# Optimization experiments

Measured on AMD Instinct MI355X. Metric: run time of the kernel, lower is better.

## Reference

```python
import jax, jax.numpy as jnp
import numpy as np

B, M, N, C, D, H, TOPK = 32, 20000, 500000, 128, 128, 4, 100
EPS = 1e-5


def setup_inputs() -> dict:
    key = jax.random.key(0)
    ks = jax.random.split(key, 24)
    f = lambda k, s: jax.random.normal(k, s, dtype=jnp.float32) * 0.05
    inp = {
        'lhs_embedding': f(ks[0], (B, C)),
        'rhs_gnn_embedding': f(ks[1], (M, C)),
        'rhs_emb_weight': f(ks[2], (N, D)),
        'proj_W': f(ks[3], (D, C)), 'proj_b': jnp.zeros((D,), jnp.float32),
        'head_W': f(ks[4], (1, C)), 'head_b': jnp.zeros((1,), jnp.float32),
        'off_emb_W': f(ks[5], (1, D)), 'off_emb_b': jnp.zeros((1,), jnp.float32),
        'off_id_W': f(ks[6], (1, D)), 'off_id_b': jnp.zeros((1,), jnp.float32),
        'Wq': f(ks[7], (D, D)), 'bq': jnp.zeros((D,), jnp.float32),
        'Wk': f(ks[8], (D, D)), 'bk': jnp.zeros((D,), jnp.float32),
        'Wv': f(ks[9], (D, D)), 'bv': jnp.zeros((D,), jnp.float32),
        'Wo': f(ks[10], (D, D)), 'bo': jnp.zeros((D,), jnp.float32),
        'ln1_g': jnp.ones((D,), jnp.float32), 'ln1_b': jnp.zeros((D,), jnp.float32),
        'ffn_W': f(ks[11], (D, D)), 'ffn_b': jnp.zeros((D,), jnp.float32),
        'ln2_g': jnp.ones((D,), jnp.float32), 'ln2_b': jnp.zeros((D,), jnp.float32),
        'rhs_idgnn_index': jax.random.randint(ks[12], (M,), 0, N, dtype=jnp.int32),
        'lhs_idgnn_batch': jnp.sort(jax.random.randint(ks[13], (M,), 0, B, dtype=jnp.int32)),
    }
    return inp


def _ln(x, g, b):
    mu = jnp.mean(x, axis=-1, keepdims=True)
    var = jnp.mean(jnp.square(x - mu), axis=-1, keepdims=True)
    return (x - mu) * jax.lax.rsqrt(var + EPS) * g + b


def reference(lhs_embedding, rhs_gnn_embedding, rhs_emb_weight, proj_W, proj_b,
              head_W, head_b, off_emb_W, off_emb_b, off_id_W, off_id_b,
              Wq, bq, Wk, bk, Wv, bv, Wo, bo, ln1_g, ln1_b, ffn_W, ffn_b,
              ln2_g, ln2_b, rhs_idgnn_index, lhs_idgnn_batch):
    # --- embgnn logits: dense [B,N] matmul + per-row offset ---
    lhs_proj = lhs_embedding @ proj_W.T + proj_b                          # [B,D]
    embgnn_logits = lhs_proj @ rhs_emb_weight.T                           # [B,N]
    embgnn_logits = embgnn_logits + (lhs_proj @ off_emb_W[0] + off_emb_b[0])[:, None]

    # --- idgnn logits on sampled rhs nodes ---
    idgnn_logits = rhs_gnn_embedding @ head_W[0] + head_b[0]              # [M]
    idgnn_logits = idgnn_logits + jnp.sum(lhs_embedding[lhs_idgnn_batch] * rhs_gnn_embedding, axis=-1)
    idgnn_offset = lhs_proj @ off_id_W[0] + off_id_b[0]                   # [B]
    idgnn_logits = idgnn_logits + idgnn_offset[lhs_idgnn_batch]

    # scatter idgnn logits into the dense logits tensor
    embgnn_logits = embgnn_logits.at[lhs_idgnn_batch, rhs_idgnn_index].set(idgnn_logits)

    # --- final rhs embeddings: shallow table + scattered GNN embeddings ---
    copy_tensor = jnp.zeros_like(rhs_emb_weight).at[rhs_idgnn_index].set(rhs_gnn_embedding)
    final_rhs_embed = rhs_emb_weight + copy_tensor                        # [N,D]

    # --- rerank: topk -> gather -> MAB -> scatter back ---
    _, topk_index = jax.lax.top_k(embgnn_logits, TOPK)                    # [B,TOPK]
    top_embed = final_rhs_embed[topk_index]                               # [B,TOPK,D]

    dh = D // H
    q = (top_embed @ Wq.T + bq).reshape(B, TOPK, H, dh)
    k = (top_embed @ Wk.T + bk).reshape(B, TOPK, H, dh)
    v = (top_embed @ Wv.T + bv).reshape(B, TOPK, H, dh)
    att = jnp.einsum('bthd,bshd->bhts', q, k) / jnp.sqrt(jnp.float32(dh))
    att = jax.nn.softmax(att, axis=-1)
    o = jnp.einsum('bhts,bshd->bthd', att, v).reshape(B, TOPK, D) @ Wo.T + bo
    x = _ln(top_embed + o, ln1_g, ln1_b)
    x = _ln(x + jax.nn.relu(x @ ffn_W.T + ffn_b), ln2_g, ln2_b)           # tr_embed [B,TOPK,D]

    # original code passes lhs_proj[lhs_idgnn_batch] and indexes rows 0..B-1
    lhs_q = lhs_proj[lhs_idgnn_batch][:B]                                 # [B,D]
    scores = jnp.sum(lhs_q[:, None, :] * x, axis=-1)                      # [B,TOPK]
    rows = jnp.arange(B)[:, None]
    transformer_logits = jnp.full((B, N), -jnp.inf, dtype=embgnn_logits.dtype)
    transformer_logits = transformer_logits.at[rows, topk_index].set(scores)

    return embgnn_logits, transformer_logits, topk_index
```

## Files before the change

kernel.cpp:

```cpp
#include <hip/hip_runtime.h>

typedef unsigned long long u64;
typedef unsigned int u32;

#define N_NODES 500000
#define M_SAMP  20000
#define BB      32
#define DD      128
#define TOPK    100
#define NBINS   2048
#define CAP     2048
#define C4PB    3907
#define LN_EPS  1e-5f
#define NEG_BIG -1.0e30f

__device__ __forceinline__ u32 fkey(float x) {
  u32 u = __float_as_uint(x);
  u32 mask = (u32)((int)u >> 31) | 0x80000000u;
  return u ^ mask;
}

__global__ void k_lhsproj(const float* __restrict__ lhs, const float* __restrict__ pW,
                          const float* __restrict__ pb, const float* __restrict__ oeW,
                          const float* __restrict__ oeb, const float* __restrict__ oiW,
                          const float* __restrict__ oib,
                          float* __restrict__ lhs_proj, float* __restrict__ lhs_projT,
                          float* __restrict__ oe_sc, float* __restrict__ oi_sc) {
  __shared__ float lrow[DD];
  __shared__ float red[DD];
  int b = blockIdx.x, d = threadIdx.x;
  lrow[d] = lhs[b * DD + d];
  __syncthreads();
  float acc = pb[d];
  for (int c = 0; c < DD; ++c) acc += lrow[c] * pW[d * DD + c];
  lhs_proj[b * DD + d] = acc;
  lhs_projT[d * BB + b] = acc;
  red[d] = acc * oeW[d];
  __syncthreads();
  for (int s = 64; s > 0; s >>= 1) { if (d < s) red[d] += red[d + s]; __syncthreads(); }
  if (d == 0) oe_sc[b] = red[0] + oeb[0];
  __syncthreads();
  red[d] = acc * oiW[d];
  __syncthreads();
  for (int s = 64; s > 0; s >>= 1) { if (d < s) red[d] += red[d + s]; __syncthreads(); }
  if (d == 0) oi_sc[b] = red[0] + oib[0];
}

__global__ void k_idgnn(const float* __restrict__ rgnn, const float* __restrict__ lhs,
                        const float* __restrict__ hW, const float* __restrict__ hb,
                        const float* __restrict__ oi_sc,
                        const int* __restrict__ ridx, const int* __restrict__ rbat,
                        float* __restrict__ val, int* __restrict__ win) {
  int wid = threadIdx.x >> 6, lane = threadIdx.x & 63;
  int m = blockIdx.x * 4 + wid;
  if (m >= M_SAMP) return;
  int b = rbat[m], n = ridx[m];
  float2 rg = ((const float2*)(rgnn + (size_t)m * DD))[lane];
  float2 hw = ((const float2*)hW)[lane];
  float2 le = ((const float2*)(lhs + (size_t)b * DD))[lane];
  float p = rg.x * hw.x + rg.y * hw.y + rg.x * le.x + rg.y * le.y;
  for (int off = 32; off > 0; off >>= 1) p += __shfl_down(p, off);
  int w = 1;
  for (int j0 = m + 1; j0 < M_SAMP; j0 += 64) {
    int j = j0 + lane;
    bool inb = (j < M_SAMP) && (rbat[j] == b);
    bool match = inb && (ridx[j] == n);
    if (__ballot(match)) { w = 0; break; }
    if (__ballot(inb) != ~0ULL) break;
  }
  if (lane == 0) { val[m] = p + hb[0] + oi_sc[b]; win[m] = w; }
}

__global__ void k_setup(int* __restrict__ inv, u32* __restrict__ hist,
                        u32* __restrict__ cand_cnt) {
  int i = blockIdx.x * 256 + threadIdx.x;
  if (i < N_NODES) inv[i] = -1;
  if (i < BB * NBINS) hist[i] = 0;
  if (i < BB) cand_cnt[i] = 0;
}

__global__ __launch_bounds__(256) void k_embgnn(const float* __restrict__ rhs,
    const float* __restrict__ lhsT, const float* __restrict__ oe_sc,
    float* __restrict__ out, float* __restrict__ tr) {
  __shared__ float sT[64][DD + 4];
  int tid = threadIdx.x;
  long n0 = (long)blockIdx.x * 64;
  #pragma unroll
  for (int p = 0; p < 8; ++p) {
    int f = p * 256 + tid;
    int r = f >> 5, c4 = (f & 31) << 2;
    long n = n0 + r; if (n >= N_NODES) n = N_NODES - 1;
    float4 v = *(const float4*)(rhs + n * DD + c4);
    sT[r][c4] = v.x; sT[r][c4 + 1] = v.y; sT[r][c4 + 2] = v.z; sT[r][c4 + 3] = v.w;
  }
  __syncthreads();
  int lane = tid & 63;
  int bg = __builtin_amdgcn_readfirstlane((tid >> 6) * 8);
  float acc[8];
  #pragma unroll
  for (int j = 0; j < 8; ++j) acc[j] = 0.f;
  const float4* srow = (const float4*)&sT[lane][0];
  #pragma unroll 4
  for (int cq = 0; cq < 32; ++cq) {
    float4 rv = srow[cq];
    const float* lp = lhsT + cq * 4 * BB + bg;
    #pragma unroll
    for (int j = 0; j < 8; ++j) {
      acc[j] += lp[j] * rv.x;
      acc[j] += lp[BB + j] * rv.y;
      acc[j] += lp[2 * BB + j] * rv.z;
      acc[j] += lp[3 * BB + j] * rv.w;
    }
  }
  long n = n0 + lane;
  if (n < N_NODES) {
    #pragma unroll
    for (int j = 0; j < 8; ++j) {
      out[(long)(bg + j) * N_NODES + n] = acc[j] + oe_sc[bg + j];
      tr[(long)(bg + j) * N_NODES + n] = NEG_BIG;
    }
  }
}

__global__ void k_scatter2(const int* __restrict__ ridx, const int* __restrict__ rbat,
                           const float* __restrict__ val, const int* __restrict__ win,
                           int* __restrict__ inv, float* __restrict__ out) {
  int m = blockIdx.x * 256 + threadIdx.x;
  if (m < M_SAMP) {
    atomicMax(&inv[ridx[m]], m);
    if (win[m]) out[(long)rbat[m] * N_NODES + ridx[m]] = val[m];
  }
}

__global__ void k_hist(const float* __restrict__ out, u32* __restrict__ hist) {
  __shared__ u32 hsh[NBINS];
  int tid = threadIdx.x;
  for (int i = tid; i < NBINS; i += 256) hsh[i] = 0;
  __syncthreads();
  int row = blockIdx.y;
  const float4* o4 = (const float4*)out + (long)row * (N_NODES / 4);
  int start = blockIdx.x * C4PB;
  int end = min(start + C4PB, N_NODES / 4);
  for (int i = start + tid; i < end; i += 256) {
    float4 v = o4[i];
    atomicAdd(&hsh[fkey(v.x) >> 21], 1u);
    atomicAdd(&hsh[fkey(v.y) >> 21], 1u);
    atomicAdd(&hsh[fkey(v.z) >> 21], 1u);
    atomicAdd(&hsh[fkey(v.w) >> 21], 1u);
  }
  __syncthreads();
  for (int i = tid; i < NBINS; i += 256)
    if (hsh[i]) atomicAdd(&hist[row * NBINS + i], hsh[i]);
}

__global__ void k_collect(const float* __restrict__ out, const u32* __restrict__ hist,
                          u32* __restrict__ cand_cnt, u64* __restrict__ cand) {
  __shared__ u32 part[256];
  __shared__ int s_cb;
  int tid = threadIdx.x, row = blockIdx.y;
  const u32* hrow = hist + row * NBINS;
  u32 p = 0;
  #pragma unroll
  for (int j = 0; j < 8; ++j) p += hrow[tid * 8 + j];
  part[tid] = p;
  __syncthreads();
  if (tid == 0) {
    u32 cum = 0; int g = 255, found = 0;
    for (; g > 0; --g) { cum += part[g]; if (cum >= TOPK) { found = 1; break; } }
    u32 c2 = found ? (cum - part[g]) : cum;
    int hi = found ? g * 8 + 7 : 7;
    int bin;
    for (bin = hi; bin > 0; --bin) { c2 += hrow[bin]; if (c2 >= TOPK) break; }
    s_cb = bin;
  }
  __syncthreads();
  u32 cb = (u32)s_cb;
  const float4* o4 = (const float4*)out + (long)row * (N_NODES / 4);
  int start = blockIdx.x * C4PB;
  int end = min(start + C4PB, N_NODES / 4);
  for (int i = start + tid; i < end; i += 256) {
    float4 v = o4[i];
    u32 kk[4] = { fkey(v.x), fkey(v.y), fkey(v.z), fkey(v.w) };
    #pragma unroll
    for (int j = 0; j < 4; ++j) {
      if ((kk[j] >> 21) >= cb) {
        u32 pos = atomicAdd(&cand_cnt[row], 1u);
        int idx = i * 4 + j;
        if (pos < CAP) cand[(long)row * CAP + pos] = ((u64)kk[j] << 32) | (u32)(~idx);
      }
    }
  }
}

__global__ __launch_bounds__(1024) void k_sort(const u64* __restrict__ cand,
                                               const u32* __restrict__ cand_cnt,
                                               int* __restrict__ topk_out) {
  __shared__ u64 sh[CAP];
  int row = blockIdx.x, tid = threadIdx.x;
  int cnt = min((int)cand_cnt[row], CAP);
  int NS = 128; while (NS < cnt) NS <<= 1;
  for (int i = tid; i < NS; i += 1024) sh[i] = (i < cnt) ? cand[(long)row * CAP + i] : 0ULL;
  __syncthreads();
  for (int k2 = 2; k2 <= NS; k2 <<= 1) {
    for (int j = k2 >> 1; j > 0; j >>= 1) {
      for (int i = tid; i < NS; i += 1024) {
        int ixj = i ^ j;
        if (ixj > i) {
          u64 a = sh[i], c = sh[ixj];
          bool up = ((i & k2) == 0);
          if (up ? (a < c) : (a > c)) { sh[i] = c; sh[ixj] = a; }
        }
      }
      __syncthreads();
    }
  }
  if (tid < TOPK) topk_out[row * TOPK + tid] = (int)(~(u32)sh[tid]);
}

__global__ __launch_bounds__(128) void k_gqkv(const int* __restrict__ topk,
    const int* __restrict__ inv, const float* __restrict__ rhs_emb,
    const float* __restrict__ rgnn,
    const float* __restrict__ Wq, const float* __restrict__ bq,
    const float* __restrict__ Wk, const float* __restrict__ bk,
    const float* __restrict__ Wv, const float* __restrict__ bv,
    float* __restrict__ x0, float* __restrict__ q, float* __restrict__ k_,
    float* __restrict__ v_) {
  __shared__ float xr[16][DD];
  __shared__ int sn[16], sm[16];
  int tid = threadIdx.x;
  long r0 = (long)blockIdx.x * 16;
  if (tid < 16) { int n = topk[r0 + tid]; sn[tid] = n; sm[tid] = inv[n]; }
  __syncthreads();
  for (int i = tid; i < 16 * DD; i += 128) {
    int r = i >> 7, dd_ = i & 127;
    int n = sn[r], mw = sm[r];
    float v = rhs_emb[(long)n * DD + dd_];
    if (mw >= 0) v += rgnn[(long)mw * DD + dd_];
    xr[r][dd_] = v;
    x0[r0 * DD + i] = v;
  }
  __syncthreads();
  float aq[16], ak[16], av[16];
  float bqv = bq[tid], bkv = bk[tid], bvv = bv[tid];
  #pragma unroll
  for (int r = 0; r < 16; ++r) { aq[r] = bqv; ak[r] = bkv; av[r] = bvv; }
  const float4* Wq4 = (const float4*)(Wq + tid * DD);
  const float4* Wk4 = (const float4*)(Wk + tid * DD);
  const float4* Wv4 = (const float4*)(Wv + tid * DD);
  #pragma unroll 4
  for (int c4 = 0; c4 < 32; ++c4) {
    float4 wq = Wq4[c4], wk = Wk4[c4], wv = Wv4[c4];
    #pragma unroll
    for (int r = 0; r < 16; ++r) {
      const float* xa = &xr[r][c4 << 2];
      float x0v = xa[0], x1v = xa[1], x2v = xa[2], x3v = xa[3];
      aq[r] += x0v * wq.x + x1v * wq.y + x2v * wq.z + x3v * wq.w;
      ak[r] += x0v * wk.x + x1v * wk.y + x2v * wk.z + x3v * wk.w;
      av[r] += x0v * wv.x + x1v * wv.y + x2v * wv.z + x3v * wv.w;
    }
  }
  #pragma unroll
  for (int r = 0; r < 16; ++r) {
    q[(r0 + r) * DD + tid] = aq[r];
    k_[(r0 + r) * DD + tid] = ak[r];
    v_[(r0 + r) * DD + tid] = av[r];
  }
}

__global__ __launch_bounds__(128) void k_att(const float* __restrict__ q,
    const float* __restrict__ k_, const float* __restrict__ v_, float* __restrict__ o) {
  __shared__ float kv[TOPK][32];
  __shared__ float att[TOPK][TOPK];
  int b = blockIdx.x >> 2, h = blockIdx.x & 3;
  int tid = threadIdx.x;
  long base = (long)b * TOPK * DD + h * 32;
  for (int i = tid; i < TOPK * 32; i += 128) {
    int t = i >> 5, d = i & 31;
    kv[t][d] = k_[base + (long)t * DD + d];
  }
  __syncthreads();
  int t = tid;
  if (t < TOPK) {
    float4 q4[8];
    const float4* qp = (const float4*)(q + base + (long)t * DD);
    #pragma unroll
    for (int i = 0; i < 8; ++i) q4[i] = qp[i];
    float qreg[32];
    #pragma unroll
    for (int i = 0; i < 8; ++i) {
      qreg[4 * i] = q4[i].x; qreg[4 * i + 1] = q4[i].y;
      qreg[4 * i + 2] = q4[i].z; qreg[4 * i + 3] = q4[i].w;
    }
    const float scale = 0.17677669529663687f;
    for (int s = 0; s < TOPK; ++s) {
      float sum = 0.f;
      #pragma unroll
      for (int d = 0; d < 32; ++d) sum += qreg[d] * kv[s][d];
      att[t][s] = sum * scale;
    }
    float mx = att[t][0];
    for (int s = 1; s < TOPK; ++s) mx = fmaxf(mx, att[t][s]);
    float sum = 0.f;
    for (int s = 0; s < TOPK; ++s) { float e = expf(att[t][s] - mx); att[t][s] = e; sum += e; }
    float inv = 1.f / sum;
    for (int s = 0; s < TOPK; ++s) att[t][s] *= inv;
  }
  __syncthreads();
  for (int i = tid; i < TOPK * 32; i += 128) {
    int tt = i >> 5, d = i & 31;
    kv[tt][d] = v_[base + (long)tt * DD + d];
  }
  __syncthreads();
  if (t < TOPK) {
    float osum[32];
    #pragma unroll
    for (int d = 0; d < 32; ++d) osum[d] = 0.f;
    for (int s = 0; s < TOPK; ++s) {
      float a = att[t][s];
      #pragma unroll
      for (int d = 0; d < 32; ++d) osum[d] += a * kv[s][d];
    }
    float4* op = (float4*)(o + base + (long)t * DD);
    #pragma unroll
    for (int i = 0; i < 8; ++i)
      op[i] = make_float4(osum[4 * i], osum[4 * i + 1], osum[4 * i + 2], osum[4 * i + 3]);
  }
}

__global__ __launch_bounds__(128) void k_xform(const float* __restrict__ ob_,
    const float* __restrict__ Wo, const float* __restrict__ bo,
    const float* __restrict__ x0, const float* __restrict__ g1,
    const float* __restrict__ be1, const float* __restrict__ fW,
    const float* __restrict__ fb, const float* __restrict__ g2,
    const float* __restrict__ be2, const float* __restrict__ lhs_proj,
    const int* __restrict__ lbat, const int* __restrict__ topk,
    float* __restrict__ tr) {
  __shared__ float sA[16][DD];
  __shared__ float sT[16][DD + 4];
  __shared__ float sMu[16], sRs[16];
  int tid = threadIdx.x;
  long r0 = (long)blockIdx.x * 16;
  for (int i = tid; i < 16 * DD; i += 128) sA[i >> 7][i & 127] = ob_[r0 * DD + i];
  __syncthreads();
  float vacc[16];
  #pragma unroll
  for (int r = 0; r < 16; ++r) vacc[r] = bo[tid];
  const float4* Wo4 = (const float4*)(Wo + tid * DD);
  #pragma unroll 4
  for (int c4 = 0; c4 < 32; ++c4) {
    float4 w = Wo4[c4];
    #pragma unroll
    for (int r = 0; r < 16; ++r) {
      const float* xa = &sA[r][c4 << 2];
      vacc[r] += xa[0] * w.x + xa[1] * w.y + xa[2] * w.z + xa[3] * w.w;
    }
  }
  float tval[16];
  #pragma unroll
  for (int r = 0; r < 16; ++r) {
    tval[r] = vacc[r] + x0[(r0 + r) * DD + tid];
    sT[r][tid] = tval[r];
  }
  __syncthreads();
  int rr = tid >> 3, sub = tid & 7;
  {
    float s = 0.f, qq = 0.f;
    const float* tp = &sT[rr][sub * 16];
    #pragma unroll
    for (int j = 0; j < 16; ++j) { float v = tp[j]; s += v; qq += v * v; }
    s += __shfl_xor(s, 1); qq += __shfl_xor(qq, 1);
    s += __shfl_xor(s, 2); qq += __shfl_xor(qq, 2);
    s += __shfl_xor(s, 4); qq += __shfl_xor(qq, 4);
    if (sub == 0) {
      float mu = s * (1.f / 128.f);
      sMu[rr] = mu;
      sRs[rr] = rsqrtf(fmaxf(qq * (1.f / 128.f) - mu * mu, 0.f) + LN_EPS);
    }
  }
  __syncthreads();
  float g1v = g1[tid], b1v = be1[tid];
  float x1v[16];
  #pragma unroll
  for (int r = 0; r < 16; ++r) {
    x1v[r] = (tval[r] - sMu[r]) * sRs[r] * g1v + b1v;
    sA[r][tid] = x1v[r];
  }
  __syncthreads();
  #pragma unroll
  for (int r = 0; r < 16; ++r) vacc[r] = fb[tid];
  const float4* fW4 = (const float4*)(fW + tid * DD);
  #pragma unroll 4
  for (int c4 = 0; c4 < 32; ++c4) {
    float4 w = fW4[c4];
    #pragma unroll
    for (int r = 0; r < 16; ++r) {
      const float* xa = &sA[r][c4 << 2];
      vacc[r] += xa[0] * w.x + xa[1] * w.y + xa[2] * w.z + xa[3] * w.w;
    }
  }
  float t2[16];
  #pragma unroll
  for (int r = 0; r < 16; ++r) { t2[r] = x1v[r] + fmaxf(vacc[r], 0.f); sT[r][tid] = t2[r]; }
  __syncthreads();
  {
    float s = 0.f, qq = 0.f;
    const float* tp = &sT[rr][sub * 16];
    #pragma unroll
    for (int j = 0; j < 16; ++j) { float v = tp[j]; s += v; qq += v * v; }
    s += __shfl_xor(s, 1); qq += __shfl_xor(qq, 1);
    s += __shfl_xor(s, 2); qq += __shfl_xor(qq, 2);
    s += __shfl_xor(s, 4); qq += __shfl_xor(qq, 4);
    if (sub == 0) {
      float mu = s * (1.f / 128.f);
      sMu[rr] = mu;
      sRs[rr] = rsqrtf(fmaxf(qq * (1.f / 128.f) - mu * mu, 0.f) + LN_EPS);
    }
  }
  __syncthreads();
  float g2v = g2[tid], b2v = be2[tid];
  #pragma unroll
  for (int r = 0; r < 16; ++r) {
    long row = r0 + r;
    int b = (int)(row / TOPK);
    float lq = lhs_proj[(long)lbat[b] * DD + tid];
    float x2 = (t2[r] - sMu[r]) * sRs[r] * g2v + b2v;
    sT[r][tid] = x2 * lq;
  }
  __syncthreads();
  {
    float s = 0.f;
    const float* tp = &sT[rr][sub * 16];
    #pragma unroll
    for (int j = 0; j < 16; ++j) s += tp[j];
    s += __shfl_xor(s, 1);
    s += __shfl_xor(s, 2);
    s += __shfl_xor(s, 4);
    if (sub == 0) {
      long row = r0 + rr;
      int b = (int)(row / TOPK);
      tr[(long)b * N_NODES + topk[row]] = s;
    }
  }
}

extern "C" void kernel_launch(void* const* d_in, const int* in_sizes, int n_in,
                              void* d_out, int out_size, void* d_ws, size_t ws_size,
                              hipStream_t stream) {
  const float* lhs_emb  = (const float*)d_in[0];
  const float* rgnn     = (const float*)d_in[1];
  const float* rhs_emb  = (const float*)d_in[2];
  const float* proj_W   = (const float*)d_in[3];
  const float* proj_b   = (const float*)d_in[4];
  const float* head_W   = (const float*)d_in[5];
  const float* head_b   = (const float*)d_in[6];
  const float* off_emb_W= (const float*)d_in[7];
  const float* off_emb_b= (const float*)d_in[8];
  const float* off_id_W = (const float*)d_in[9];
  const float* off_id_b = (const float*)d_in[10];
  const float* Wq = (const float*)d_in[11]; const float* bq = (const float*)d_in[12];
  const float* Wk = (const float*)d_in[13]; const float* bk = (const float*)d_in[14];
  const float* Wv = (const float*)d_in[15]; const float* bv = (const float*)d_in[16];
  const float* Wo = (const float*)d_in[17]; const float* bo = (const float*)d_in[18];
  const float* ln1_g = (const float*)d_in[19]; const float* ln1_b = (const float*)d_in[20];
  const float* ffn_W = (const float*)d_in[21]; const float* ffn_b = (const float*)d_in[22];
  const float* ln2_g = (const float*)d_in[23]; const float* ln2_b = (const float*)d_in[24];
  const int* ridx = (const int*)d_in[25];
  const int* rbat = (const int*)d_in[26];

  float* out_emb = (float*)d_out;
  float* out_tr  = out_emb + (long)BB * N_NODES;
  int*   out_topk = (int*)(out_emb + 2L * BB * N_NODES);

  char* w = (char*)d_ws;
  float* lhs_proj  = (float*)w; w += 16384;
  float* lhs_projT = (float*)w; w += 16384;
  float* oe_sc    = (float*)w; w += 128;
  float* oi_sc    = (float*)w; w += 128;
  float* idval    = (float*)w; w += 80000;
  int*   idwin    = (int*)w;   w += 80000;
  int*   inv      = (int*)w;   w += 2000000;
  u32*   hist     = (u32*)w;   w += BB * NBINS * 4;
  u32*   cand_cnt = (u32*)w;   w += 128;
  u64*   cand     = (u64*)w;   w += (long)BB * CAP * 8;
  float* x0 = (float*)w; w += 1638400;
  float* qb = (float*)w; w += 1638400;
  float* kb = (float*)w; w += 1638400;
  float* vb = (float*)w; w += 1638400;
  float* ob = (float*)w; w += 1638400;

  k_lhsproj<<<32, 128, 0, stream>>>(lhs_emb, proj_W, proj_b, off_emb_W, off_emb_b,
                                    off_id_W, off_id_b, lhs_proj, lhs_projT, oe_sc, oi_sc);
  k_idgnn<<<M_SAMP / 4, 256, 0, stream>>>(rgnn, lhs_emb, head_W, head_b, oi_sc,
                                          ridx, rbat, idval, idwin);
  k_setup<<<(N_NODES + 255) / 256, 256, 0, stream>>>(inv, hist, cand_cnt);
  k_embgnn<<<(N_NODES + 63) / 64, 256, 0, stream>>>(rhs_emb, lhs_projT, oe_sc,
                                                    out_emb, out_tr);
  k_scatter2<<<(M_SAMP + 255) / 256, 256, 0, stream>>>(ridx, rbat, idval, idwin,
                                                       inv, out_emb);
  k_hist<<<dim3(32, BB), 256, 0, stream>>>(out_emb, hist);
  k_collect<<<dim3(32, BB), 256, 0, stream>>>(out_emb, hist, cand_cnt, cand);
  k_sort<<<BB, 1024, 0, stream>>>(cand, cand_cnt, out_topk);

  k_gqkv<<<BB * TOPK / 16, 128, 0, stream>>>(out_topk, inv, rhs_emb, rgnn,
                                             Wq, bq, Wk, bk, Wv, bv, x0, qb, kb, vb);
  k_att<<<BB * 4, 128, 0, stream>>>(qb, kb, vb, ob);
  k_xform<<<BB * TOPK / 16, 128, 0, stream>>>(ob, Wo, bo, x0, ln1_g, ln1_b,
                                              ffn_W, ffn_b, ln2_g, ln2_b,
                                              lhs_proj, rbat, out_topk, out_tr);
}
```

Baseline: 328.4 us.

## Fuse front kernels, merge candidate collect with sort, recompute x0 in xform

Three setup kernels (lhs projection, idgnn scoring and buffer init) become one launch, split by block index. Because the projection blocks now run alongside the idgnn blocks, the oi offset is added later in the scatter kernel. The candidate collect and bitonic sort kernels become one kernel per row that gathers candidates directly into shared memory, removing the global candidate buffer and counter. k_xform rebuilds the residual input from rhs_emb/rgnn instead of reading a stored x0 buffer. The cost is that each row's full scan for candidates now runs in a single 1024-thread block instead of 32 blocks, which reduces parallelism in that pass.

```diff
diff --git a/kernel.cpp b/kernel.cpp
--- a/kernel.cpp
+++ b/kernel.cpp
@@ -20,63 +20,64 @@
   return u ^ mask;
 }
 
-__global__ void k_lhsproj(const float* __restrict__ lhs, const float* __restrict__ pW,
-                          const float* __restrict__ pb, const float* __restrict__ oeW,
-                          const float* __restrict__ oeb, const float* __restrict__ oiW,
-                          const float* __restrict__ oib,
-                          float* __restrict__ lhs_proj, float* __restrict__ lhs_projT,
-                          float* __restrict__ oe_sc, float* __restrict__ oi_sc) {
-  __shared__ float lrow[DD];
-  __shared__ float red[DD];
-  int b = blockIdx.x, d = threadIdx.x;
-  lrow[d] = lhs[b * DD + d];
-  __syncthreads();
-  float acc = pb[d];
-  for (int c = 0; c < DD; ++c) acc += lrow[c] * pW[d * DD + c];
-  lhs_proj[b * DD + d] = acc;
-  lhs_projT[d * BB + b] = acc;
-  red[d] = acc * oeW[d];
-  __syncthreads();
-  for (int s = 64; s > 0; s >>= 1) { if (d < s) red[d] += red[d + s]; __syncthreads(); }
-  if (d == 0) oe_sc[b] = red[0] + oeb[0];
-  __syncthreads();
-  red[d] = acc * oiW[d];
-  __syncthreads();
-  for (int s = 64; s > 0; s >>= 1) { if (d < s) red[d] += red[d + s]; __syncthreads(); }
-  if (d == 0) oi_sc[b] = red[0] + oib[0];
-}
-
-__global__ void k_idgnn(const float* __restrict__ rgnn, const float* __restrict__ lhs,
-                        const float* __restrict__ hW, const float* __restrict__ hb,
-                        const float* __restrict__ oi_sc,
-                        const int* __restrict__ ridx, const int* __restrict__ rbat,
-                        float* __restrict__ val, int* __restrict__ win) {
-  int wid = threadIdx.x >> 6, lane = threadIdx.x & 63;
-  int m = blockIdx.x * 4 + wid;
-  if (m >= M_SAMP) return;
-  int b = rbat[m], n = ridx[m];
-  float2 rg = ((const float2*)(rgnn + (size_t)m * DD))[lane];
-  float2 hw = ((const float2*)hW)[lane];
-  float2 le = ((const float2*)(lhs + (size_t)b * DD))[lane];
-  float p = rg.x * hw.x + rg.y * hw.y + rg.x * le.x + rg.y * le.y;
-  for (int off = 32; off > 0; off >>= 1) p += __shfl_down(p, off);
-  int w = 1;
-  for (int j0 = m + 1; j0 < M_SAMP; j0 += 64) {
-    int j = j0 + lane;
-    bool inb = (j < M_SAMP) && (rbat[j] == b);
-    bool match = inb && (ridx[j] == n);
-    if (__ballot(match)) { w = 0; break; }
-    if (__ballot(inb) != ~0ULL) break;
-  }
-  if (lane == 0) { val[m] = p + hb[0] + oi_sc[b]; win[m] = w; }
-}
-
-__global__ void k_setup(int* __restrict__ inv, u32* __restrict__ hist,
-                        u32* __restrict__ cand_cnt) {
-  int i = blockIdx.x * 256 + threadIdx.x;
-  if (i < N_NODES) inv[i] = -1;
-  if (i < BB * NBINS) hist[i] = 0;
-  if (i < BB) cand_cnt[i] = 0;
+__global__ __launch_bounds__(256) void k_front(
+    const float* __restrict__ lhs, const float* __restrict__ pW,
+    const float* __restrict__ pb, const float* __restrict__ oeW,
+    const float* __restrict__ oeb, const float* __restrict__ oiW,
+    const float* __restrict__ oib, const float* __restrict__ rgnn,
+    const float* __restrict__ hW, const float* __restrict__ hb,
+    const int* __restrict__ ridx, const int* __restrict__ rbat,
+    float* __restrict__ lhs_proj, float* __restrict__ lhs_projT,
+    float* __restrict__ oe_sc, float* __restrict__ oi_sc,
+    float* __restrict__ val, int* __restrict__ win,
+    int* __restrict__ inv, u32* __restrict__ hist) {
+  int bid = blockIdx.x, tid = threadIdx.x;
+  if (bid < 32) {
+    __shared__ float lrow[DD];
+    __shared__ float red[DD];
+    int b = bid, d = tid;
+    if (d < DD) lrow[d] = lhs[b * DD + d];
+    __syncthreads();
+    float acc = 0.f;
+    if (d < DD) {
+      acc = pb[d];
+      for (int c = 0; c < DD; ++c) acc += lrow[c] * pW[d * DD + c];
+      lhs_proj[b * DD + d] = acc;
+      lhs_projT[d * BB + b] = acc;
+      red[d] = acc * oeW[d];
+    }
+    __syncthreads();
+    for (int s = 64; s > 0; s >>= 1) { if (d < s) red[d] += red[d + s]; __syncthreads(); }
+    if (d == 0) oe_sc[b] = red[0] + oeb[0];
+    __syncthreads();
+    if (d < DD) red[d] = acc * oiW[d];
+    __syncthreads();
+    for (int s = 64; s > 0; s >>= 1) { if (d < s) red[d] += red[d + s]; __syncthreads(); }
+    if (d == 0) oi_sc[b] = red[0] + oib[0];
+  } else if (bid < 32 + M_SAMP / 4) {
+    int wid = tid >> 6, lane = tid & 63;
+    int m = (bid - 32) * 4 + wid;
+    if (m >= M_SAMP) return;
+    int b = rbat[m], n = ridx[m];
+    float2 rg = ((const float2*)(rgnn + (size_t)m * DD))[lane];
+    float2 hw = ((const float2*)hW)[lane];
+    float2 le = ((const float2*)(lhs + (size_t)b * DD))[lane];
+    float p = rg.x * hw.x + rg.y * hw.y + rg.x * le.x + rg.y * le.y;
+    for (int off = 32; off > 0; off >>= 1) p += __shfl_down(p, off);
+    int w = 1;
+    for (int j0 = m + 1; j0 < M_SAMP; j0 += 64) {
+      int j = j0 + lane;
+      bool inb = (j < M_SAMP) && (rbat[j] == b);
+      bool match = inb && (ridx[j] == n);
+      if (__ballot(match)) { w = 0; break; }
+      if (__ballot(inb) != ~0ULL) break;
+    }
+    if (lane == 0) { val[m] = p + hb[0]; win[m] = w; }
+  } else {
+    int i = (bid - (32 + M_SAMP / 4)) * 256 + tid;
+    if (i < N_NODES) inv[i] = -1;
+    if (i < BB * NBINS) hist[i] = 0;
+  }
 }
 
 __global__ __launch_bounds__(256) void k_embgnn(const float* __restrict__ rhs,
@@ -124,11 +125,15 @@
 
 __global__ void k_scatter2(const int* __restrict__ ridx, const int* __restrict__ rbat,
                            const float* __restrict__ val, const int* __restrict__ win,
+                           const float* __restrict__ oi_sc,
                            int* __restrict__ inv, float* __restrict__ out) {
   int m = blockIdx.x * 256 + threadIdx.x;
   if (m < M_SAMP) {
     atomicMax(&inv[ridx[m]], m);
-    if (win[m]) out[(long)rbat[m] * N_NODES + ridx[m]] = val[m];
+    if (win[m]) {
+      int b = rbat[m];
+      out[(long)b * N_NODES + ridx[m]] = val[m] + oi_sc[b];
+    }
   }
 }
 
@@ -153,16 +158,22 @@
     if (hsh[i]) atomicAdd(&hist[row * NBINS + i], hsh[i]);
 }
 
-__global__ void k_collect(const float* __restrict__ out, const u32* __restrict__ hist,
-                          u32* __restrict__ cand_cnt, u64* __restrict__ cand) {
+__global__ __launch_bounds__(1024) void k_topk(const float* __restrict__ out,
+                                               const u32* __restrict__ hist,
+                                               int* __restrict__ topk_out) {
+  __shared__ u64 sh[CAP];
   __shared__ u32 part[256];
   __shared__ int s_cb;
-  int tid = threadIdx.x, row = blockIdx.y;
+  __shared__ u32 s_cnt;
+  int tid = threadIdx.x, row = blockIdx.x;
   const u32* hrow = hist + row * NBINS;
-  u32 p = 0;
-  #pragma unroll
-  for (int j = 0; j < 8; ++j) p += hrow[tid * 8 + j];
-  part[tid] = p;
+  if (tid < 256) {
+    u32 p = 0;
+    #pragma unroll
+    for (int j = 0; j < 8; ++j) p += hrow[tid * 8 + j];
+    part[tid] = p;
+  }
+  if (tid == 0) s_cnt = 0;
   __syncthreads();
   if (tid == 0) {
     u32 cum = 0; int g = 255, found = 0;
@@ -176,30 +187,22 @@
   __syncthreads();
   u32 cb = (u32)s_cb;
   const float4* o4 = (const float4*)out + (long)row * (N_NODES / 4);
-  int start = blockIdx.x * C4PB;
-  int end = min(start + C4PB, N_NODES / 4);
-  for (int i = start + tid; i < end; i += 256) {
+  for (int i = tid; i < N_NODES / 4; i += 1024) {
     float4 v = o4[i];
     u32 kk[4] = { fkey(v.x), fkey(v.y), fkey(v.z), fkey(v.w) };
     #pragma unroll
     for (int j = 0; j < 4; ++j) {
       if ((kk[j] >> 21) >= cb) {
-        u32 pos = atomicAdd(&cand_cnt[row], 1u);
+        u32 pos = atomicAdd(&s_cnt, 1u);
         int idx = i * 4 + j;
-        if (pos < CAP) cand[(long)row * CAP + pos] = ((u64)kk[j] << 32) | (u32)(~idx);
+        if (pos < CAP) sh[pos] = ((u64)kk[j] << 32) | (u32)(~idx);
       }
     }
   }
-}
-
-__global__ __launch_bounds__(1024) void k_sort(const u64* __restrict__ cand,
-                                               const u32* __restrict__ cand_cnt,
-                                               int* __restrict__ topk_out) {
-  __shared__ u64 sh[CAP];
-  int row = blockIdx.x, tid = threadIdx.x;
-  int cnt = min((int)cand_cnt[row], CAP);
+  __syncthreads();
+  int cnt = min((int)s_cnt, CAP);
   int NS = 128; while (NS < cnt) NS <<= 1;
-  for (int i = tid; i < NS; i += 1024) sh[i] = (i < cnt) ? cand[(long)row * CAP + i] : 0ULL;
+  for (int i = cnt + tid; i < NS; i += 1024) sh[i] = 0ULL;
   __syncthreads();
   for (int k2 = 2; k2 <= NS; k2 <<= 1) {
     for (int j = k2 >> 1; j > 0; j >>= 1) {
@@ -223,8 +226,7 @@
     const float* __restrict__ Wq, const float* __restrict__ bq,
     const float* __restrict__ Wk, const float* __restrict__ bk,
     const float* __restrict__ Wv, const float* __restrict__ bv,
-    float* __restrict__ x0, float* __restrict__ q, float* __restrict__ k_,
-    float* __restrict__ v_) {
+    float* __restrict__ q, float* __restrict__ k_, float* __restrict__ v_) {
   __shared__ float xr[16][DD];
   __shared__ int sn[16], sm[16];
   int tid = threadIdx.x;
@@ -237,7 +239,6 @@
     float v = rhs_emb[(long)n * DD + dd_];
     if (mw >= 0) v += rgnn[(long)mw * DD + dd_];
     xr[r][dd_] = v;
-    x0[r0 * DD + i] = v;
   }
   __syncthreads();
   float aq[16], ak[16], av[16];
@@ -329,17 +330,20 @@
 
 __global__ __launch_bounds__(128) void k_xform(const float* __restrict__ ob_,
     const float* __restrict__ Wo, const float* __restrict__ bo,
-    const float* __restrict__ x0, const float* __restrict__ g1,
-    const float* __restrict__ be1, const float* __restrict__ fW,
-    const float* __restrict__ fb, const float* __restrict__ g2,
-    const float* __restrict__ be2, const float* __restrict__ lhs_proj,
-    const int* __restrict__ lbat, const int* __restrict__ topk,
+    const int* __restrict__ topk, const int* __restrict__ inv,
+    const float* __restrict__ rhs_emb, const float* __restrict__ rgnn,
+    const float* __restrict__ g1, const float* __restrict__ be1,
+    const float* __restrict__ fW, const float* __restrict__ fb,
+    const float* __restrict__ g2, const float* __restrict__ be2,
+    const float* __restrict__ lhs_proj, const int* __restrict__ lbat,
     float* __restrict__ tr) {
   __shared__ float sA[16][DD];
   __shared__ float sT[16][DD + 4];
   __shared__ float sMu[16], sRs[16];
+  __shared__ int sn[16], sm[16];
   int tid = threadIdx.x;
   long r0 = (long)blockIdx.x * 16;
+  if (tid < 16) { int n = topk[r0 + tid]; sn[tid] = n; sm[tid] = inv[n]; }
   for (int i = tid; i < 16 * DD; i += 128) sA[i >> 7][i & 127] = ob_[r0 * DD + i];
   __syncthreads();
   float vacc[16];
@@ -358,7 +362,9 @@
   float tval[16];
   #pragma unroll
   for (int r = 0; r < 16; ++r) {
-    tval[r] = vacc[r] + x0[(r0 + r) * DD + tid];
+    float x0v = rhs_emb[(long)sn[r] * DD + tid];
+    if (sm[r] >= 0) x0v += rgnn[(long)sm[r] * DD + tid];
+    tval[r] = vacc[r] + x0v;
     sT[r][tid] = tval[r];
   }
   __syncthreads();
@@ -480,31 +486,28 @@
   int*   idwin    = (int*)w;   w += 80000;
   int*   inv      = (int*)w;   w += 2000000;
   u32*   hist     = (u32*)w;   w += BB * NBINS * 4;
-  u32*   cand_cnt = (u32*)w;   w += 128;
-  u64*   cand     = (u64*)w;   w += (long)BB * CAP * 8;
-  float* x0 = (float*)w; w += 1638400;
   float* qb = (float*)w; w += 1638400;
   float* kb = (float*)w; w += 1638400;
   float* vb = (float*)w; w += 1638400;
   float* ob = (float*)w; w += 1638400;
 
-  k_lhsproj<<<32, 128, 0, stream>>>(lhs_emb, proj_W, proj_b, off_emb_W, off_emb_b,
-                                    off_id_W, off_id_b, lhs_proj, lhs_projT, oe_sc, oi_sc);
-  k_idgnn<<<M_SAMP / 4, 256, 0, stream>>>(rgnn, lhs_emb, head_W, head_b, oi_sc,
-                                          ridx, rbat, idval, idwin);
-  k_setup<<<(N_NODES + 255) / 256, 256, 0, stream>>>(inv, hist, cand_cnt);
+  const int SETUP_BLKS = (N_NODES + 255) / 256;
+  k_front<<<32 + M_SAMP / 4 + SETUP_BLKS, 256, 0, stream>>>(
+      lhs_emb, proj_W, proj_b, off_emb_W, off_emb_b, off_id_W, off_id_b,
+      rgnn, head_W, head_b, ridx, rbat,
+      lhs_proj, lhs_projT, oe_sc, oi_sc, idval, idwin, inv, hist);
   k_embgnn<<<(N_NODES + 63) / 64, 256, 0, stream>>>(rhs_emb, lhs_projT, oe_sc,
                                                     out_emb, out_tr);
   k_scatter2<<<(M_SAMP + 255) / 256, 256, 0, stream>>>(ridx, rbat, idval, idwin,
-                                                       inv, out_emb);
+                                                       oi_sc, inv, out_emb);
   k_hist<<<dim3(32, BB), 256, 0, stream>>>(out_emb, hist);
-  k_collect<<<dim3(32, BB), 256, 0, stream>>>(out_emb, hist, cand_cnt, cand);
-  k_sort<<<BB, 1024, 0, stream>>>(cand, cand_cnt, out_topk);
+  k_topk<<<BB, 1024, 0, stream>>>(out_emb, hist, out_topk);
 
   k_gqkv<<<BB * TOPK / 16, 128, 0, stream>>>(out_topk, inv, rhs_emb, rgnn,
-                                             Wq, bq, Wk, bk, Wv, bv, x0, qb, kb, vb);
+                                             Wq, bq, Wk, bk, Wv, bv, qb, kb, vb);
   k_att<<<BB * 4, 128, 0, stream>>>(qb, kb, vb, ob);
-  k_xform<<<BB * TOPK / 16, 128, 0, stream>>>(ob, Wo, bo, x0, ln1_g, ln1_b,
+  k_xform<<<BB * TOPK / 16, 128, 0, stream>>>(ob, Wo, bo, out_topk, inv,
+                                              rhs_emb, rgnn, ln1_g, ln1_b,
                                               ffn_W, ffn_b, ln2_g, ln2_b,
-                                              lhs_proj, rbat, out_topk, out_tr);
-}
+                                              lhs_proj, rbat, out_tr);
+}
```

After: 312.1 us. 5.0% less time.
